# Optimization experiments

Measured on AMD Instinct MI355X. Metric: run time of the kernel, lower is better.

The kernel has to match this reference:

```python
import jax, jax.numpy as jnp
import numpy as np

N = 50000
E = 400000
D_IN = 128
D_OUT = 128
D_NODE = 6
EPS = 1e-5


def _layernorm(h, g, b):
    mu = jnp.mean(h, axis=-1, keepdims=True)
    var = jnp.var(h, axis=-1, keepdims=True)
    return (h - mu) * jax.lax.rsqrt(var + EPS) * g + b


def setup_inputs() -> dict:
    key = jax.random.key(0)
    ks = jax.random.split(key, 8)
    d_cat = 3 * D_IN + 2 * D_NODE  # 396 = input_dim*3 + 12
    return {
        "x": jax.random.normal(ks[0], (N, D_NODE), jnp.float32),
        "edge_index": jax.random.randint(ks[1], (2, E), 0, N, dtype=jnp.int32),
        "edge_attr": jax.random.normal(ks[2], (E, D_IN), jnp.float32),
        "mask": (jax.random.uniform(ks[3], (E,)) > 0.5).astype(jnp.float32),
        "num_nodes": N,
        "W_edge": jax.random.normal(ks[4], (d_cat, D_OUT), jnp.float32) / np.sqrt(d_cat).astype(np.float32),
        "b_edge": jnp.zeros((D_OUT,), jnp.float32),
        "W1": jax.random.normal(ks[5], (D_OUT, 2 * D_OUT), jnp.float32) / np.sqrt(D_OUT).astype(np.float32),
        "b1": jnp.zeros((2 * D_OUT,), jnp.float32),
        "W2": jax.random.normal(ks[6], (2 * D_OUT, D_OUT), jnp.float32) / np.sqrt(2 * D_OUT).astype(np.float32),
        "b2": jnp.zeros((D_OUT,), jnp.float32),
        "g1": jnp.ones((D_OUT,), jnp.float32),
        "be1": jnp.zeros((D_OUT,), jnp.float32),
        "g2": jnp.ones((D_OUT,), jnp.float32),
        "be2": jnp.zeros((D_OUT,), jnp.float32),
    }


def reference(x, edge_attr, mask, W_edge, b_edge, W1, b1, W2, b2, g1, be1, g2, be2, edge_index, num_nodes):
    row, col = edge_index[0], edge_index[1]
    # mean-like aggregation of incoming edge features onto destination nodes
    agg = jax.ops.segment_sum(edge_attr * mask[:, None], col, num_segments=num_nodes)  # [N, D_IN]
    den = jax.ops.segment_sum(mask, col, num_segments=num_nodes) + 1.0  # [N]
    node_rep = jnp.concatenate([agg / den[:, None], x], axis=1)  # [N, D_IN + D_NODE]
    edge_rep = jnp.concatenate([node_rep[row], node_rep[col], edge_attr], axis=-1)  # [E, 3*D_IN+12]
    h = _layernorm(edge_attr[:, :D_OUT] + edge_rep @ W_edge + b_edge, g1, be1)  # [E, D_OUT]
    out = _layernorm(h + jax.nn.relu(h @ W1 + b1) @ W2 + b2, g2, be2)  # [E, D_OUT]
    return (node_rep, out)
```

## Files before the change

### kernel.cpp

```cpp
#include <hip/hip_runtime.h>


constexpr int NN = 50000;
constexpr int NE = 400000;
constexpr int DI = 128;
constexpr int DN = 6;
constexpr int DR = 134;
constexpr float LN_EPS = 1e-5f;

using f4 = __attribute__((ext_vector_type(4))) float;
using s8 = __attribute__((ext_vector_type(8))) short;

__device__ __forceinline__ unsigned short f2bf(float f) {
    unsigned u = __float_as_uint(f);
    u += 0x7fff + ((u >> 16) & 1);
    return (unsigned short)(u >> 16);
}

__device__ __forceinline__ float bf2f(unsigned short b) {
    return __uint_as_float((unsigned)b << 16);
}

__device__ __forceinline__ float red16(float v) {
    int x;
    x = __builtin_amdgcn_update_dpp(0, __float_as_int(v), 0x121, 0xf, 0xf, true);
    v += __int_as_float(x);
    x = __builtin_amdgcn_update_dpp(0, __float_as_int(v), 0x122, 0xf, 0xf, true);
    v += __int_as_float(x);
    x = __builtin_amdgcn_update_dpp(0, __float_as_int(v), 0x124, 0xf, 0xf, true);
    v += __int_as_float(x);
    x = __builtin_amdgcn_update_dpp(0, __float_as_int(v), 0x128, 0xf, 0xf, true);
    v += __int_as_float(x);
    return v;
}

__global__ __launch_bounds__(256) void deg_kernel(
    const float* __restrict__ mask, const int* __restrict__ ei,
    int* __restrict__ deg)
{
    int e = blockIdx.x * 256 + threadIdx.x;
    if (e >= NE) return;
    if (mask[e] != 0.f) atomicAdd(&deg[ei[NE + e]], 1);
}

__global__ __launch_bounds__(1024) void scan_kernel(
    const int* __restrict__ deg, int* __restrict__ offs, int* __restrict__ cursor)
{
    __shared__ int part[1024];
    const int t = threadIdx.x;
    constexpr int CH = (NN + 1023) / 1024;
    const int base = t * CH;
    const int lim  = min(base + CH, NN);

    int s = 0;
    for (int i = base; i < lim; ++i) s += deg[i];
    part[t] = s;
    __syncthreads();
    for (int off = 1; off < 1024; off <<= 1) {
        int add = (t >= off) ? part[t - off] : 0;
        __syncthreads();
        part[t] += add;
        __syncthreads();
    }
    int run = (t == 0) ? 0 : part[t - 1];
    for (int i = base; i < lim; ++i) {
        offs[i]   = run;
        cursor[i] = run;
        run += deg[i];
    }
    if (t == 1023) offs[NN] = part[1023];
}

__global__ __launch_bounds__(256) void binfill_kernel(
    const float* __restrict__ mask, const int* __restrict__ ei,
    int* __restrict__ cursor, int* __restrict__ bucket)
{
    int e = blockIdx.x * 256 + threadIdx.x;
    if (e >= NE) return;
    if (mask[e] != 0.f) {
        int pos = atomicAdd(&cursor[ei[NE + e]], 1);
        bucket[pos] = e;
    }
}

__global__ __launch_bounds__(256) void gather_kernel(
    const float* __restrict__ edge_attr, const float* __restrict__ mask,
    const float* __restrict__ x, const int* __restrict__ offs,
    const int* __restrict__ bucket, float* __restrict__ node_out)
{
    int n = blockIdx.x * 4 + (threadIdx.x >> 6);
    if (n >= NN) return;
    const int lane = threadIdx.x & 63;
    const int beg = offs[n], end = offs[n + 1];
    float2 acc = make_float2(0.f, 0.f);
    float den = 0.f;
    for (int j = beg; j < end; ++j) {
        int e = bucket[j];
        float m = mask[e];
        float2 v = *reinterpret_cast<const float2*>(edge_attr + (size_t)e * 128 + lane * 2);
        acc.x += v.x * m;
        acc.y += v.y * m;
        den   += m;
    }
    float inv = 1.f / (den + 1.f);
    float2 o = make_float2(acc.x * inv, acc.y * inv);
    *reinterpret_cast<float2*>(node_out + (size_t)n * DR + lane * 2) = o;
    if (lane < DN) node_out[(size_t)n * DR + DI + lane] = x[n * DN + lane];
}

__global__ __launch_bounds__(256) void prep_w_kernel(
    const float* __restrict__ W_edge, const float* __restrict__ W1,
    const float* __restrict__ W2,
    unsigned short* __restrict__ WcT, unsigned short* __restrict__ W1T,
    unsigned short* __restrict__ W2T)
{
    int idx = blockIdx.x * 256 + threadIdx.x;
    if (idx < 16384) {
        int n = idx >> 7, k = idx & 127;
        float v = W_edge[(268 + k) * 128 + n] + (k == n ? 1.f : 0.f);
        WcT[n * 128 + k] = f2bf(v);
    } else if (idx < 49152) {
        int j = idx - 16384;
        int n = j >> 7, k = j & 127;
        W1T[n * 128 + k] = f2bf(W1[k * 256 + n]);
    } else if (idx < 81920) {
        int j = idx - 49152;
        int n = j >> 8, k = j & 255;
        W2T[n * 256 + k] = f2bf(W2[k * 128 + n]);
    }
}

__global__ __launch_bounds__(256) void pq_kernel(
    const float* __restrict__ nr, const float* __restrict__ W_edge,
    const float* __restrict__ b_edge,
    float* __restrict__ P, float* __restrict__ Q)
{
    __shared__ float As[32 * 136];
    const int t = threadIdx.x;
    const int n0 = blockIdx.x * 32;

    for (int idx = t; idx < 32 * 136; idx += 256) {
        int n = idx / 136, k = idx - n * 136;
        float v = 0.f;
        if (n0 + n < NN && k < DR) v = nr[(size_t)(n0 + n) * DR + k];
        As[idx] = v;
    }
    __syncthreads();

    const int et = t >> 5, jt = t & 31;
    float4 accP[4], accQ[4];
    #pragma unroll
    for (int i = 0; i < 4; ++i) {
        accP[i] = make_float4(0.f, 0.f, 0.f, 0.f);
        accQ[i] = make_float4(0.f, 0.f, 0.f, 0.f);
    }
    for (int k0 = 0; k0 < 136; k0 += 4) {
        float4 wa[4], wb[4];
        #pragma unroll
        for (int d = 0; d < 4; ++d) {
            wa[d] = *reinterpret_cast<const float4*>(&W_edge[(size_t)(k0 + d) * 128 + 4 * jt]);
            wb[d] = *reinterpret_cast<const float4*>(&W_edge[(size_t)(134 + k0 + d) * 128 + 4 * jt]);
        }
        #pragma unroll
        for (int i = 0; i < 4; ++i) {
            float4 a4 = *reinterpret_cast<const float4*>(&As[(4 * et + i) * 136 + k0]);
            accP[i].x += a4.x * wa[0].x + a4.y * wa[1].x + a4.z * wa[2].x + a4.w * wa[3].x;
            accP[i].y += a4.x * wa[0].y + a4.y * wa[1].y + a4.z * wa[2].y + a4.w * wa[3].y;
            accP[i].z += a4.x * wa[0].z + a4.y * wa[1].z + a4.z * wa[2].z + a4.w * wa[3].z;
            accP[i].w += a4.x * wa[0].w + a4.y * wa[1].w + a4.z * wa[2].w + a4.w * wa[3].w;
            accQ[i].x += a4.x * wb[0].x + a4.y * wb[1].x + a4.z * wb[2].x + a4.w * wb[3].x;
            accQ[i].y += a4.x * wb[0].y + a4.y * wb[1].y + a4.z * wb[2].y + a4.w * wb[3].y;
            accQ[i].z += a4.x * wb[0].z + a4.y * wb[1].z + a4.z * wb[2].z + a4.w * wb[3].z;
            accQ[i].w += a4.x * wb[0].w + a4.y * wb[1].w + a4.z * wb[2].w + a4.w * wb[3].w;
        }
    }
    float4 bev = *reinterpret_cast<const float4*>(&b_edge[4 * jt]);
    #pragma unroll
    for (int i = 0; i < 4; ++i) {
        int n = n0 + 4 * et + i;
        if (n < NN) {
            float4 p = accP[i];
            p.x += bev.x; p.y += bev.y; p.z += bev.z; p.w += bev.w;
            *reinterpret_cast<float4*>(&P[(size_t)n * 128 + 4 * jt]) = p;
            *reinterpret_cast<float4*>(&Q[(size_t)n * 128 + 4 * jt]) = accQ[i];
        }
    }
}

constexpr int PA = 136;
constexpr int PU = 264;
constexpr int ET = 64;
constexpr int NTILE = NE / ET;

__global__ __launch_bounds__(1024, 4) void ffn_kernel(
    const float* __restrict__ edge_attr,
    const int* __restrict__ ei,
    const float* __restrict__ P,
    const float* __restrict__ Q,
    const unsigned short* __restrict__ WcT,
    const unsigned short* __restrict__ W1T,
    const unsigned short* __restrict__ W2T,
    const float* __restrict__ b1, const float* __restrict__ b2,
    const float* __restrict__ g1, const float* __restrict__ be1,
    const float* __restrict__ g2, const float* __restrict__ be2,
    float* __restrict__ out)
{
    __shared__ short lds_a[ET * PA];
    __shared__ short lds_u[ET * PU];
    __shared__ float red_part[2][8][32][2];
    __shared__ float musig[2][ET][2];

    const int t    = threadIdx.x;
    const int w    = t >> 6;
    const int lane = t & 63;
    const int q    = lane >> 4;
    const int c    = lane & 15;
    const int mg   = w >> 3;
    const int cw   = w & 7;

    s8 wcf[4], w1f[2][4], w2f[8];
    #pragma unroll
    for (int k0 = 0; k0 < 4; ++k0)
        wcf[k0] = *reinterpret_cast<const s8*>(WcT + (cw * 16 + c) * 128 + k0 * 32 + q * 8);
    #pragma unroll
    for (int nt = 0; nt < 2; ++nt)
        #pragma unroll
        for (int k0 = 0; k0 < 4; ++k0)
            w1f[nt][k0] = *reinterpret_cast<const s8*>(W1T + (cw * 32 + nt * 16 + c) * 128 + k0 * 32 + q * 8);
    #pragma unroll
    for (int k0 = 0; k0 < 8; ++k0)
        w2f[k0] = *reinterpret_cast<const s8*>(W2T + (cw * 16 + c) * 256 + k0 * 32 + q * 8);

    const float g1c  = g1[cw * 16 + c],  be1c = be1[cw * 16 + c];
    const float b1v0 = b1[cw * 32 + c],  b1v1 = b1[cw * 32 + 16 + c];
    const float b2c  = b2[cw * 16 + c];
    const float g2c  = g2[cw * 16 + c],  be2c = be2[cw * 16 + c];

    const int srow = t >> 4;
    const int sti  = t & 15;

    for (int tile = blockIdx.x; tile < NTILE; tile += gridDim.x) {
        const int e0 = tile * ET;

        {
            const float4* src = reinterpret_cast<const float4*>(
                edge_attr + (size_t)(e0 + srow) * 128 + sti * 8);
            float4 v0 = src[0], v1 = src[1];
            s8 bb;
            bb[0] = (short)f2bf(v0.x); bb[1] = (short)f2bf(v0.y);
            bb[2] = (short)f2bf(v0.z); bb[3] = (short)f2bf(v0.w);
            bb[4] = (short)f2bf(v1.x); bb[5] = (short)f2bf(v1.y);
            bb[6] = (short)f2bf(v1.z); bb[7] = (short)f2bf(v1.w);
            *reinterpret_cast<s8*>(&lds_a[srow * PA + sti * 8]) = bb;
        }
        __syncthreads();

        f4 acc1[2];
        acc1[0] = {0.f, 0.f, 0.f, 0.f};
        acc1[1] = {0.f, 0.f, 0.f, 0.f};
        #pragma unroll
        for (int k0 = 0; k0 < 4; ++k0)
            #pragma unroll
            for (int mt = 0; mt < 2; ++mt) {
                s8 a = *reinterpret_cast<const s8*>(&lds_a[(mg * 32 + mt * 16 + c) * PA + k0 * 32 + q * 8]);
                acc1[mt] = __builtin_amdgcn_mfma_f32_16x16x32_bf16(a, wcf[k0], acc1[mt], 0, 0, 0);
            }

        #pragma unroll
        for (int mt = 0; mt < 2; ++mt)
            #pragma unroll
            for (int reg = 0; reg < 4; ++reg) {
                int e  = e0 + mg * 32 + mt * 16 + q * 4 + reg;
                int er = ei[e], ec = ei[NE + e];
                acc1[mt][reg] += P[(size_t)er * 128 + cw * 16 + c]
                               + Q[(size_t)ec * 128 + cw * 16 + c];
            }

        #pragma unroll
        for (int mt = 0; mt < 2; ++mt)
            #pragma unroll
            for (int reg = 0; reg < 4; ++reg) {
                float v  = acc1[mt][reg];
                float sv = red16(v);
                float sq = red16(v * v);
                if (c == 0) {
                    int r = mt * 16 + q * 4 + reg;
                    float2 p2; p2.x = sv; p2.y = sq;
                    *reinterpret_cast<float2*>(&red_part[mg][cw][r][0]) = p2;
                }
            }
        __syncthreads();
        if (t < ET) {
            float s = 0.f, ss = 0.f;
            #pragma unroll
            for (int i = 0; i < 8; ++i) {
                float2 p2 = *reinterpret_cast<const float2*>(&red_part[t >> 5][i][t & 31][0]);
                s += p2.x; ss += p2.y;
            }
            float mu  = s * (1.f / 128.f);
            float var = ss * (1.f / 128.f) - mu * mu;
            float2 m2; m2.x = mu; m2.y = rsqrtf(var + LN_EPS);
            *reinterpret_cast<float2*>(&musig[0][t][0]) = m2;
        }
        __syncthreads();

        #pragma unroll
        for (int mt = 0; mt < 2; ++mt)
            #pragma unroll
            for (int reg = 0; reg < 4; ++reg) {
                int r = mg * 32 + mt * 16 + q * 4 + reg;
                float2 m2 = *reinterpret_cast<const float2*>(&musig[0][r][0]);
                float h = (acc1[mt][reg] - m2.x) * m2.y * g1c + be1c;
                lds_a[r * PA + cw * 16 + c] = (short)f2bf(h);
            }
        __syncthreads();

        f4 acc2[2][2];
        acc2[0][0] = {0.f,0.f,0.f,0.f}; acc2[0][1] = {0.f,0.f,0.f,0.f};
        acc2[1][0] = {0.f,0.f,0.f,0.f}; acc2[1][1] = {0.f,0.f,0.f,0.f};
        #pragma unroll
        for (int k0 = 0; k0 < 4; ++k0)
            #pragma unroll
            for (int mt = 0; mt < 2; ++mt) {
                s8 a = *reinterpret_cast<const s8*>(&lds_a[(mg * 32 + mt * 16 + c) * PA + k0 * 32 + q * 8]);
                acc2[mt][0] = __builtin_amdgcn_mfma_f32_16x16x32_bf16(a, w1f[0][k0], acc2[mt][0], 0, 0, 0);
                acc2[mt][1] = __builtin_amdgcn_mfma_f32_16x16x32_bf16(a, w1f[1][k0], acc2[mt][1], 0, 0, 0);
            }
        #pragma unroll
        for (int mt = 0; mt < 2; ++mt)
            #pragma unroll
            for (int reg = 0; reg < 4; ++reg) {
                int r = mg * 32 + mt * 16 + q * 4 + reg;
                float u0 = fmaxf(acc2[mt][0][reg] + b1v0, 0.f);
                float u1 = fmaxf(acc2[mt][1][reg] + b1v1, 0.f);
                lds_u[r * PU + cw * 32 + c]      = (short)f2bf(u0);
                lds_u[r * PU + cw * 32 + 16 + c] = (short)f2bf(u1);
            }
        __syncthreads();

        f4 acc3[2];
        #pragma unroll
        for (int mt = 0; mt < 2; ++mt)
            #pragma unroll
            for (int reg = 0; reg < 4; ++reg) {
                int r = mg * 32 + mt * 16 + q * 4 + reg;
                acc3[mt][reg] = bf2f((unsigned short)lds_a[r * PA + cw * 16 + c]) + b2c;
            }
        #pragma unroll
        for (int k0 = 0; k0 < 8; ++k0)
            #pragma unroll
            for (int mt = 0; mt < 2; ++mt) {
                s8 a = *reinterpret_cast<const s8*>(&lds_u[(mg * 32 + mt * 16 + c) * PU + k0 * 32 + q * 8]);
                acc3[mt] = __builtin_amdgcn_mfma_f32_16x16x32_bf16(a, w2f[k0], acc3[mt], 0, 0, 0);
            }

        #pragma unroll
        for (int mt = 0; mt < 2; ++mt)
            #pragma unroll
            for (int reg = 0; reg < 4; ++reg) {
                float v  = acc3[mt][reg];
                float sv = red16(v);
                float sq = red16(v * v);
                if (c == 0) {
                    int r = mt * 16 + q * 4 + reg;
                    float2 p2; p2.x = sv; p2.y = sq;
                    *reinterpret_cast<float2*>(&red_part[mg][cw][r][0]) = p2;
                }
            }
        __syncthreads();
        if (t < ET) {
            float s = 0.f, ss = 0.f;
            #pragma unroll
            for (int i = 0; i < 8; ++i) {
                float2 p2 = *reinterpret_cast<const float2*>(&red_part[t >> 5][i][t & 31][0]);
                s += p2.x; ss += p2.y;
            }
            float mu  = s * (1.f / 128.f);
            float var = ss * (1.f / 128.f) - mu * mu;
            float2 m2; m2.x = mu; m2.y = rsqrtf(var + LN_EPS);
            *reinterpret_cast<float2*>(&musig[1][t][0]) = m2;
        }
        __syncthreads();

        #pragma unroll
        for (int mt = 0; mt < 2; ++mt)
            #pragma unroll
            for (int reg = 0; reg < 4; ++reg) {
                int r = mg * 32 + mt * 16 + q * 4 + reg;
                float2 m2 = *reinterpret_cast<const float2*>(&musig[1][r][0]);
                float o = (acc3[mt][reg] - m2.x) * m2.y * g2c + be2c;
                out[(size_t)(e0 + r) * 128 + cw * 16 + c] = o;
            }
    }
}

extern "C" void kernel_launch(void* const* d_in, const int* in_sizes, int n_in,
                              void* d_out, int out_size, void* d_ws, size_t ws_size,
                              hipStream_t stream) {
    const float* x         = (const float*)d_in[0];
    const int*   ei        = (const int*)  d_in[1];
    const float* edge_attr = (const float*)d_in[2];
    const float* mask      = (const float*)d_in[3];
    const float* W_edge    = (const float*)d_in[5];
    const float* b_edge    = (const float*)d_in[6];
    const float* W1        = (const float*)d_in[7];
    const float* b1        = (const float*)d_in[8];
    const float* W2        = (const float*)d_in[9];
    const float* b2        = (const float*)d_in[10];
    const float* g1        = (const float*)d_in[11];
    const float* be1       = (const float*)d_in[12];
    const float* g2        = (const float*)d_in[13];
    const float* be2       = (const float*)d_in[14];

    float* node_out  = (float*)d_out;
    float* out_edges = (float*)d_out + (size_t)NN * DR;

    char* ws = (char*)d_ws;
    int*            deg    = (int*)(ws);
    int*            offs   = (int*)(ws + (256 << 10));
    int*            cursor = (int*)(ws + (512 << 10));
    unsigned short* WcT    = (unsigned short*)(ws + (768 << 10));
    unsigned short* W1T    = (unsigned short*)(ws + (768 << 10) + 32768);
    unsigned short* W2T    = (unsigned short*)(ws + (768 << 10) + 98304);
    int*            bucket = (int*)(ws + (1 << 20));
    float*          P      = (float*)(ws + (1 << 20));
    float*          Q      = (float*)(ws + (1 << 20) + 26214400);

    hipMemsetAsync(deg, 0, (size_t)NN * sizeof(int), stream);

    deg_kernel<<<(NE + 255) / 256, 256, 0, stream>>>(mask, ei, deg);
    scan_kernel<<<1, 1024, 0, stream>>>(deg, offs, cursor);
    binfill_kernel<<<(NE + 255) / 256, 256, 0, stream>>>(mask, ei, cursor, bucket);
    gather_kernel<<<(NN + 3) / 4, 256, 0, stream>>>(edge_attr, mask, x, offs, bucket, node_out);
    prep_w_kernel<<<320, 256, 0, stream>>>(W_edge, W1, W2, WcT, W1T, W2T);
    pq_kernel<<<(NN + 31) / 32, 256, 0, stream>>>(node_out, W_edge, b_edge, P, Q);
    ffn_kernel<<<256, 1024, 0, stream>>>(edge_attr, ei, P, Q, WcT, W1T, W2T,
                                         b1, b2, g1, be1, g2, be2, out_edges);
}
```

Before: 866.7 us.

## Store P/Q projections in fp16, widen gather and pq tiles

The per-node projections P and Q are now stored as fp16 instead of fp32, which halves the bytes of the random row gathers in the edge FFN kernel. The gather kernel drops the mask reads because the buckets already hold only masked edges. It splits each node's edges across two half-waves using float4 loads and takes the denominator from the bucket count. The pq kernel tile grows from 32 to 64 nodes per block to reuse the weight loads more. The cost is fp16 rounding error in P and Q before the layernorm.

```diff
diff --git a/kernel.cpp b/kernel.cpp
--- a/kernel.cpp
+++ b/kernel.cpp
@@ -1,5 +1,7 @@
 #include <hip/hip_runtime.h>
 
+
+#include <hip/hip_fp16.h>
 
 constexpr int NN = 50000;
 constexpr int NE = 400000;
@@ -10,6 +12,7 @@
 
 using f4 = __attribute__((ext_vector_type(4))) float;
 using s8 = __attribute__((ext_vector_type(8))) short;
+using h4 = __attribute__((ext_vector_type(4))) _Float16;
 
 __device__ __forceinline__ unsigned short f2bf(float f) {
     unsigned u = __float_as_uint(f);
@@ -84,27 +87,35 @@
 }
 
 __global__ __launch_bounds__(256) void gather_kernel(
-    const float* __restrict__ edge_attr, const float* __restrict__ mask,
-    const float* __restrict__ x, const int* __restrict__ offs,
-    const int* __restrict__ bucket, float* __restrict__ node_out)
+    const float* __restrict__ edge_attr, const float* __restrict__ x,
+    const int* __restrict__ offs, const int* __restrict__ bucket,
+    float* __restrict__ node_out)
 {
     int n = blockIdx.x * 4 + (threadIdx.x >> 6);
     if (n >= NN) return;
     const int lane = threadIdx.x & 63;
+    const int half = lane >> 5;
+    const int sl   = lane & 31;
     const int beg = offs[n], end = offs[n + 1];
-    float2 acc = make_float2(0.f, 0.f);
-    float den = 0.f;
-    for (int j = beg; j < end; ++j) {
+
+    float4 acc = make_float4(0.f, 0.f, 0.f, 0.f);
+    for (int j = beg + half; j < end; j += 2) {
         int e = bucket[j];
-        float m = mask[e];
-        float2 v = *reinterpret_cast<const float2*>(edge_attr + (size_t)e * 128 + lane * 2);
-        acc.x += v.x * m;
-        acc.y += v.y * m;
-        den   += m;
-    }
-    float inv = 1.f / (den + 1.f);
-    float2 o = make_float2(acc.x * inv, acc.y * inv);
-    *reinterpret_cast<float2*>(node_out + (size_t)n * DR + lane * 2) = o;
+        float4 v = reinterpret_cast<const float4*>(edge_attr)[(size_t)e * 32 + sl];
+        acc.x += v.x; acc.y += v.y; acc.z += v.z; acc.w += v.w;
+    }
+    acc.x += __shfl_xor(acc.x, 32, 64);
+    acc.y += __shfl_xor(acc.y, 32, 64);
+    acc.z += __shfl_xor(acc.z, 32, 64);
+    acc.w += __shfl_xor(acc.w, 32, 64);
+
+    float inv = 1.f / (float)(end - beg + 1);
+    if (half == 0) {
+        float2 o0 = make_float2(acc.x * inv, acc.y * inv);
+        float2 o1 = make_float2(acc.z * inv, acc.w * inv);
+        *reinterpret_cast<float2*>(node_out + (size_t)n * DR + sl * 4)     = o0;
+        *reinterpret_cast<float2*>(node_out + (size_t)n * DR + sl * 4 + 2) = o1;
+    }
     if (lane < DN) node_out[(size_t)n * DR + DI + lane] = x[n * DN + lane];
 }
 
@@ -133,13 +144,13 @@
 __global__ __launch_bounds__(256) void pq_kernel(
     const float* __restrict__ nr, const float* __restrict__ W_edge,
     const float* __restrict__ b_edge,
-    float* __restrict__ P, float* __restrict__ Q)
-{
-    __shared__ float As[32 * 136];
+    _Float16* __restrict__ P, _Float16* __restrict__ Q)
+{
+    __shared__ float As[64 * 136];
     const int t = threadIdx.x;
-    const int n0 = blockIdx.x * 32;
-
-    for (int idx = t; idx < 32 * 136; idx += 256) {
+    const int n0 = blockIdx.x * 64;
+
+    for (int idx = t; idx < 64 * 136; idx += 256) {
         int n = idx / 136, k = idx - n * 136;
         float v = 0.f;
         if (n0 + n < NN && k < DR) v = nr[(size_t)(n0 + n) * DR + k];
@@ -148,9 +159,9 @@
     __syncthreads();
 
     const int et = t >> 5, jt = t & 31;
-    float4 accP[4], accQ[4];
+    float4 accP[8], accQ[8];
     #pragma unroll
-    for (int i = 0; i < 4; ++i) {
+    for (int i = 0; i < 8; ++i) {
         accP[i] = make_float4(0.f, 0.f, 0.f, 0.f);
         accQ[i] = make_float4(0.f, 0.f, 0.f, 0.f);
     }
@@ -162,8 +173,8 @@
             wb[d] = *reinterpret_cast<const float4*>(&W_edge[(size_t)(134 + k0 + d) * 128 + 4 * jt]);
         }
         #pragma unroll
-        for (int i = 0; i < 4; ++i) {
-            float4 a4 = *reinterpret_cast<const float4*>(&As[(4 * et + i) * 136 + k0]);
+        for (int i = 0; i < 8; ++i) {
+            float4 a4 = *reinterpret_cast<const float4*>(&As[(8 * et + i) * 136 + k0]);
             accP[i].x += a4.x * wa[0].x + a4.y * wa[1].x + a4.z * wa[2].x + a4.w * wa[3].x;
             accP[i].y += a4.x * wa[0].y + a4.y * wa[1].y + a4.z * wa[2].y + a4.w * wa[3].y;
             accP[i].z += a4.x * wa[0].z + a4.y * wa[1].z + a4.z * wa[2].z + a4.w * wa[3].z;
@@ -176,13 +187,20 @@
     }
     float4 bev = *reinterpret_cast<const float4*>(&b_edge[4 * jt]);
     #pragma unroll
-    for (int i = 0; i < 4; ++i) {
-        int n = n0 + 4 * et + i;
+    for (int i = 0; i < 8; ++i) {
+        int n = n0 + 8 * et + i;
         if (n < NN) {
-            float4 p = accP[i];
-            p.x += bev.x; p.y += bev.y; p.z += bev.z; p.w += bev.w;
-            *reinterpret_cast<float4*>(&P[(size_t)n * 128 + 4 * jt]) = p;
-            *reinterpret_cast<float4*>(&Q[(size_t)n * 128 + 4 * jt]) = accQ[i];
+            h4 hp, hq;
+            hp[0] = (_Float16)(accP[i].x + bev.x);
+            hp[1] = (_Float16)(accP[i].y + bev.y);
+            hp[2] = (_Float16)(accP[i].z + bev.z);
+            hp[3] = (_Float16)(accP[i].w + bev.w);
+            hq[0] = (_Float16)accQ[i].x;
+            hq[1] = (_Float16)accQ[i].y;
+            hq[2] = (_Float16)accQ[i].z;
+            hq[3] = (_Float16)accQ[i].w;
+            *reinterpret_cast<h4*>(&P[(size_t)n * 128 + 4 * jt]) = hp;
+            *reinterpret_cast<h4*>(&Q[(size_t)n * 128 + 4 * jt]) = hq;
         }
     }
 }
@@ -191,12 +209,13 @@
 constexpr int PU = 264;
 constexpr int ET = 64;
 constexpr int NTILE = NE / ET;
+constexpr int FFN_GRID = 256;
 
 __global__ __launch_bounds__(1024, 4) void ffn_kernel(
     const float* __restrict__ edge_attr,
     const int* __restrict__ ei,
-    const float* __restrict__ P,
-    const float* __restrict__ Q,
+    const _Float16* __restrict__ P,
+    const _Float16* __restrict__ Q,
     const unsigned short* __restrict__ WcT,
     const unsigned short* __restrict__ W1T,
     const unsigned short* __restrict__ W2T,
@@ -272,8 +291,8 @@
             for (int reg = 0; reg < 4; ++reg) {
                 int e  = e0 + mg * 32 + mt * 16 + q * 4 + reg;
                 int er = ei[e], ec = ei[NE + e];
-                acc1[mt][reg] += P[(size_t)er * 128 + cw * 16 + c]
-                               + Q[(size_t)ec * 128 + cw * 16 + c];
+                acc1[mt][reg] += (float)P[(size_t)er * 128 + cw * 16 + c]
+                               + (float)Q[(size_t)ec * 128 + cw * 16 + c];
             }
 
         #pragma unroll
@@ -423,17 +442,17 @@
     unsigned short* W1T    = (unsigned short*)(ws + (768 << 10) + 32768);
     unsigned short* W2T    = (unsigned short*)(ws + (768 << 10) + 98304);
     int*            bucket = (int*)(ws + (1 << 20));
-    float*          P      = (float*)(ws + (1 << 20));
-    float*          Q      = (float*)(ws + (1 << 20) + 26214400);
+    _Float16*       P      = (_Float16*)(ws + (1 << 20));
+    _Float16*       Q      = (_Float16*)(ws + (1 << 20) + 13631488);
 
     hipMemsetAsync(deg, 0, (size_t)NN * sizeof(int), stream);
 
     deg_kernel<<<(NE + 255) / 256, 256, 0, stream>>>(mask, ei, deg);
     scan_kernel<<<1, 1024, 0, stream>>>(deg, offs, cursor);
     binfill_kernel<<<(NE + 255) / 256, 256, 0, stream>>>(mask, ei, cursor, bucket);
-    gather_kernel<<<(NN + 3) / 4, 256, 0, stream>>>(edge_attr, mask, x, offs, bucket, node_out);
+    gather_kernel<<<(NN + 3) / 4, 256, 0, stream>>>(edge_attr, x, offs, bucket, node_out);
     prep_w_kernel<<<320, 256, 0, stream>>>(W_edge, W1, W2, WcT, W1T, W2T);
-    pq_kernel<<<(NN + 31) / 32, 256, 0, stream>>>(node_out, W_edge, b_edge, P, Q);
-    ffn_kernel<<<256, 1024, 0, stream>>>(edge_attr, ei, P, Q, WcT, W1T, W2T,
-                                         b1, b2, g1, be1, g2, be2, out_edges);
-}
+    pq_kernel<<<(NN + 63) / 64, 256, 0, stream>>>(node_out, W_edge, b_edge, P, Q);
+    ffn_kernel<<<FFN_GRID, 1024, 0, stream>>>(edge_attr, ei, P, Q, WcT, W1T, W2T,
+                                              b1, b2, g1, be1, g2, be2, out_edges);
+}
```

After: 848.0 us. -2.2%, faster.
